# Performance work log

Measured on AMD Instinct MI355X. Metric: run time of the kernel, lower is better.

The kernel has to match this reference:

```python
import jax, jax.numpy as jnp
import numpy as np

EPS = 1e-5  # torch LayerNorm default


def _layernorm_hd(t, gamma, beta):
    # Normalize jointly over the last two axes (n_heads, head_dim),
    # matching nn.LayerNorm((n_heads, head_dim)).
    mu = jnp.mean(t, axis=(-2, -1), keepdims=True)
    var = jnp.var(t, axis=(-2, -1), keepdims=True)
    return (t - mu) * jax.lax.rsqrt(var + EPS) * gamma + beta


def setup_inputs() -> dict:
    key = jax.random.key(0)
    B, Hs, Ws, C = 4, 256, 256, 128  # batch, spatial grid, hidden_channels
    n_heads, head_dim = 4, C // 4
    scale = (C ** 2) / n_heads  # hidden_channels**2 / n_heads, as in __init__
    ks = jax.random.split(key, 4)
    X = jax.random.normal(ks[0], (B, Hs, Ws, C), dtype=jnp.float32)
    Wq = jax.random.normal(ks[1], (C, n_heads, head_dim), dtype=jnp.float32) / scale
    Wk = jax.random.normal(ks[2], (C, n_heads, head_dim), dtype=jnp.float32) / scale
    Wv = jax.random.normal(ks[3], (C, n_heads, head_dim), dtype=jnp.float32) / scale
    # NOTE: original forward applies layernorm_key to BOTH key and value
    # (layernorm_value params are unused); we replicate that exactly.
    gamma_k = jnp.ones((n_heads, head_dim), dtype=jnp.float32)
    beta_k = jnp.zeros((n_heads, head_dim), dtype=jnp.float32)
    return {"X": X, "Wq": Wq, "Wk": Wk, "Wv": Wv, "gamma_k": gamma_k, "beta_k": beta_k}


def reference(X, Wq, Wk, Wv, gamma_k, beta_k):
    # X: [B, Hs, Ws, C]; W*: [C, h, d]
    q = jnp.einsum('bxyc,chd->bxyhd', X, Wq)
    k = jnp.einsum('bxyc,chd->bxyhd', X, Wk)
    v = jnp.einsum('bxyc,chd->bxyhd', X, Wv)
    k = _layernorm_hd(k, gamma_k, beta_k)
    v = _layernorm_hd(v, gamma_k, beta_k)  # faithful: layernorm_key used for value too
    num_points = X.shape[1] * X.shape[2]
    kv = jnp.einsum('bxyhd,bxyhe->bhde', k, v)          # tiny [B,h,d,d]
    sa = jnp.einsum('bxyhd,bhde->bxyeh', q, kv)          # note output order (e, h)
    sa = (sa / num_points).reshape(X.shape)
    return sa
```

## Files before the change

kernel.cpp:

```cpp
#include <hip/hip_runtime.h>

#define HW 65536
#define CH 128
#define NHEADS 4
#define HDIM 32
#define EPS 1e-5f
#define INV_NP (1.0f / 65536.0f)
#define INV_C (1.0f / 128.0f)

typedef float v4f __attribute__((ext_vector_type(4)));
typedef short v8s __attribute__((ext_vector_type(8)));
typedef unsigned int v4u __attribute__((ext_vector_type(4)));

__device__ __forceinline__ ushort f2bf(float f) {
    uint u = __float_as_uint(f);
    return (ushort)((u + 0x7FFFu + ((u >> 16) & 1u)) >> 16);
}

__device__ __forceinline__ uint cvtpk(float lo, float hi) {
    uint r;
    asm("v_cvt_pk_bf16_f32 %0, %1, %2" : "=v"(r) : "v"(lo), "v"(hi));
    return r;
}

__device__ __forceinline__ v8s pack8(const float4& a, const float4& b) {
    union { uint u[4]; v8s s; } r;
    r.u[0] = cvtpk(a.x, a.y);
    r.u[1] = cvtpk(a.z, a.w);
    r.u[2] = cvtpk(b.x, b.y);
    r.u[3] = cvtpk(b.z, b.w);
    return r.s;
}

template<int CTRL>
__device__ __forceinline__ float dppadd(float x) {
    return x + __int_as_float(
        __builtin_amdgcn_mov_dpp(__float_as_int(x), CTRL, 0xF, 0xF, true));
}
__device__ __forceinline__ float red16(float x) {
    x = dppadd<0xB1>(x);
    x = dppadd<0x4E>(x);
    x = dppadd<0x141>(x);
    x = dppadd<0x140>(x);
    return x;
}

#define MFMA(a, b, c) __builtin_amdgcn_mfma_f32_16x16x32_bf16((a), (b), (c), 0, 0, 0)


__global__ __launch_bounds__(256) void prep_kernel(const float* __restrict__ Wk,
                                                   const float* __restrict__ Wv,
                                                   ushort* __restrict__ SWkT,
                                                   ushort* __restrict__ SWvT,
                                                   float* __restrict__ kv_g) {
    const int t = blockIdx.x * 256 + threadIdx.x;
    kv_g[t] = 0.f;
    kv_g[t + 8192] = 0.f;
#pragma unroll
    for (int i = 0; i < 2; ++i) {
        const int e = i * 8192 + t;
        const int c = e >> 7;
        const int row = e & 127;
        const int dst = row * 128 + (((c >> 3) + row) & 15) * 8 + (c & 7);
        SWkT[dst] = f2bf(Wk[e]);
        SWvT[dst] = f2bf(Wv[e]);
    }
}

__global__ __launch_bounds__(256, 2) void kv_kernel(const float* __restrict__ X,
                                                    const ushort* __restrict__ SWkT,
                                                    const ushort* __restrict__ SWvT,
                                                    const float* __restrict__ gamma,
                                                    const float* __restrict__ beta,
                                                    float* __restrict__ kv_g) {
    __shared__ ushort lds[40960];
    const int tid  = threadIdx.x;
    const int lane = tid & 63;
    const int w    = tid >> 6;
    const int q    = lane >> 4;
    const int ln   = lane & 15;

    const int batch  = blockIdx.x >> 7;
    const int blocal = blockIdx.x & 127;
    const float* Xb = X + ((size_t)batch * HW + (size_t)blocal * 512) * CH;

    {
        const v4u* sk = (const v4u*)SWkT;
        const v4u* sv = (const v4u*)SWvT;
        v4u* dk = (v4u*)lds;
        v4u* dv = (v4u*)(lds + 16384);
#pragma unroll
        for (int n = 0; n < 8; ++n) {
            dk[n * 256 + tid] = sk[n * 256 + tid];
            dv[n * 256 + tid] = sv[n * 256 + tid];
        }
    }

    float g8[8], be8[8];
#pragma unroll
    for (int ct = 0; ct < 8; ++ct) {
        g8[ct]  = gamma[ct * 16 + ln];
        be8[ct] = beta[ct * 16 + ln];
    }

    int brow[8];
#pragma unroll
    for (int ct = 0; ct < 8; ++ct) brow[ct] = (ct * 16 + ln) * 128;
    int bks[4];
#pragma unroll
    for (int ks = 0; ks < 4; ++ks) bks[ks] = ((ks * 4 + q + ln) & 15) * 8;
    int soff[8];
#pragma unroll
    for (int ct = 0; ct < 8; ++ct) {
        const int chn  = ct * 16 + ln;
        const int slot = (((w & 1) << 1) + (q >> 1) + chn) & 3;
        soff[ct] = chn * 32 + slot * 8 + (q & 1) * 4;
    }
    const int r0 = w * 32 + ln;
    const int r1 = r0 + 16;
    const int koff0 = r0 * 32 + ((q + r0) & 3) * 8;
    const int koff1 = r1 * 32 + ((q + r1) & 3) * 8;

    v4f kv00 = {0.f, 0.f, 0.f, 0.f}, kv01 = kv00, kv10 = kv00, kv11 = kv00;

    const float* xbase = Xb + (w * 16 + ln) * CH + q * 8;
    float4 xa[8];
#pragma unroll
    for (int ks = 0; ks < 4; ++ks) {
        xa[2 * ks]     = *(const float4*)(xbase + ks * 32);
        xa[2 * ks + 1] = *(const float4*)(xbase + ks * 32 + 4);
    }
    __syncthreads();

    v8s A[4];
#pragma unroll
    for (int ks = 0; ks < 4; ++ks) A[ks] = pack8(xa[2 * ks], xa[2 * ks + 1]);

    for (int t = 0; t < 8; ++t) {
        if (t < 7) {
            const float* xp = xbase + (size_t)(t + 1) * 64 * CH;
#pragma unroll
            for (int ks = 0; ks < 4; ++ks) {
                xa[2 * ks]     = *(const float4*)(xp + ks * 32);
                xa[2 * ks + 1] = *(const float4*)(xp + ks * 32 + 4);
            }
        }

        v4f ak[8], av[8];
#pragma unroll
        for (int ct = 0; ct < 8; ++ct) {
            ak[ct] = (v4f){0.f, 0.f, 0.f, 0.f};
            av[ct] = (v4f){0.f, 0.f, 0.f, 0.f};
        }
#pragma unroll
        for (int ks = 0; ks < 4; ++ks) {
#pragma unroll
            for (int ct = 0; ct < 8; ++ct) {
                const int kb = brow[ct] + bks[ks];
                const v8s Bk = *(const v8s*)(lds + kb);
                const v8s Bv = *(const v8s*)(lds + 16384 + kb);
                ak[ct] = MFMA(A[ks], Bk, ak[ct]);
                av[ct] = MFMA(A[ks], Bv, av[ct]);
            }
        }

        float rsk[4], rsv[4], mrk[4], mrv[4];
#pragma unroll
        for (int r = 0; r < 4; ++r) {
            float sk = 0.f, qk = 0.f, sv = 0.f, qv = 0.f;
#pragma unroll
            for (int ct = 0; ct < 8; ++ct) {
                sk += ak[ct][r]; qk = fmaf(ak[ct][r], ak[ct][r], qk);
                sv += av[ct][r]; qv = fmaf(av[ct][r], av[ct][r], qv);
            }
            sk = red16(sk); qk = red16(qk);
            sv = red16(sv); qv = red16(qv);
            const float mk = sk * INV_C, mv = sv * INV_C;
            const float rk = __builtin_amdgcn_rsqf(fmaf(qk, INV_C, -mk * mk) + EPS);
            const float rv = __builtin_amdgcn_rsqf(fmaf(qv, INV_C, -mv * mv) + EPS);
            rsk[r] = rk; mrk[r] = mk * rk;
            rsv[r] = rv; mrv[r] = mv * rv;
        }

#pragma unroll
        for (int rnd = 0; rnd < 2; ++rnd) {
            if ((w >> 1) == rnd) {
#pragma unroll
                for (int ct = 0; ct < 8; ++ct) {
#pragma unroll
                    for (int r = 0; r < 4; r += 2) {
                        const float k0 = fmaf(fmaf(ak[ct][r],     rsk[r],     -mrk[r]),     g8[ct], be8[ct]);
                        const float k1 = fmaf(fmaf(ak[ct][r + 1], rsk[r + 1], -mrk[r + 1]), g8[ct], be8[ct]);
                        const float v0 = fmaf(fmaf(av[ct][r],     rsv[r],     -mrv[r]),     g8[ct], be8[ct]);
                        const float v1 = fmaf(fmaf(av[ct][r + 1], rsv[r + 1], -mrv[r + 1]), g8[ct], be8[ct]);
                        *(uint*)(lds + 32768 + soff[ct] + r) = cvtpk(k0, k1);
                        *(uint*)(lds + 36864 + soff[ct] + r) = cvtpk(v0, v1);
                    }
                }
            }
            __syncthreads();
            {
                const v8s Ad0 = *(const v8s*)(lds + 32768 + koff0);
                const v8s Ad1 = *(const v8s*)(lds + 32768 + koff1);
                const v8s Be0 = *(const v8s*)(lds + 36864 + koff0);
                const v8s Be1 = *(const v8s*)(lds + 36864 + koff1);
                kv00 = MFMA(Ad0, Be0, kv00);
                kv01 = MFMA(Ad0, Be1, kv01);
                kv10 = MFMA(Ad1, Be0, kv10);
                kv11 = MFMA(Ad1, Be1, kv11);
            }
            __syncthreads();
        }

        if (t < 7) {
#pragma unroll
            for (int ks = 0; ks < 4; ++ks) A[ks] = pack8(xa[2 * ks], xa[2 * ks + 1]);
        }
    }

    float* dst = kv_g + (batch * NHEADS + w) * (HDIM * HDIM);
#pragma unroll
    for (int dt = 0; dt < 2; ++dt)
#pragma unroll
        for (int et = 0; et < 2; ++et) {
            const v4f f = dt == 0 ? (et == 0 ? kv00 : kv01) : (et == 0 ? kv10 : kv11);
#pragma unroll
            for (int r = 0; r < 4; ++r) {
                const int d = dt * 16 + q * 4 + r;
                const int e = et * 16 + ln;
                atomicAdd(&dst[d * HDIM + e], f[r]);
            }
        }
}

__global__ __launch_bounds__(256) void weff_kernel(const float* __restrict__ Wq,
                                                   const float* __restrict__ kv_g,
                                                   ushort* __restrict__ SWeffT) {
    const int b = blockIdx.x >> 4;
    const int part = blockIdx.x & 15;
    const int base = part * 1024 + threadIdx.x * 4;
    const int c = base >> 7;
    const int o0 = base & 127;
    const float* kvb = kv_g + b * (NHEADS * HDIM * HDIM);
#pragma unroll
    for (int n = 0; n < 4; ++n) {
        const int o = o0 + n;
        const int h = o & 3;
        const int e = o >> 2;
        float s = 0.f;
#pragma unroll
        for (int d = 0; d < HDIM; ++d)
            s += Wq[c * CH + h * HDIM + d] * kvb[h * (HDIM * HDIM) + d * HDIM + e];
        SWeffT[b * (CH * CH) + o * 128 + (((c >> 3) + o) & 15) * 8 + (c & 7)] = f2bf(s * INV_NP);
    }
}

__global__ __launch_bounds__(256, 4) void out_kernel(const float* __restrict__ X,
                                                     const ushort* __restrict__ SWeffT,
                                                     float* __restrict__ out) {
    __shared__ ushort lds[16384];
    const int tid  = threadIdx.x;
    const int lane = tid & 63;
    const int w    = tid >> 6;
    const int q    = lane >> 4;
    const int ln   = lane & 15;

    const int batch  = blockIdx.x >> 8;
    const int blocal = blockIdx.x & 255;
    const size_t p0 = (size_t)batch * HW + (size_t)blocal * 256;

    {
        const v4u* s = (const v4u*)(SWeffT + batch * (CH * CH));
        v4u* d = (v4u*)lds;
#pragma unroll
        for (int n = 0; n < 8; ++n) d[n * 256 + tid] = s[n * 256 + tid];
    }

    int arow[8];
#pragma unroll
    for (int ot = 0; ot < 8; ++ot) arow[ot] = (ot * 16 + ln) * 128;
    int aks[4];
#pragma unroll
    for (int ks = 0; ks < 4; ++ks) aks[ks] = ((ks * 4 + q + ln) & 15) * 8;

    const float* xbase = X + (p0 + w * 16 + ln) * CH + q * 8;
    float* obase       = out + (p0 + w * 16 + ln) * CH + q * 4;

    float4 xa[8];
#pragma unroll
    for (int ks = 0; ks < 4; ++ks) {
        xa[2 * ks]     = *(const float4*)(xbase + ks * 32);
        xa[2 * ks + 1] = *(const float4*)(xbase + ks * 32 + 4);
    }
    __syncthreads();

    v8s Bx[4];
#pragma unroll
    for (int ks = 0; ks < 4; ++ks) Bx[ks] = pack8(xa[2 * ks], xa[2 * ks + 1]);

    for (int t = 0; t < 4; ++t) {
        if (t < 3) {
            const float* xp = xbase + (size_t)(t + 1) * 64 * CH;
#pragma unroll
            for (int ks = 0; ks < 4; ++ks) {
                xa[2 * ks]     = *(const float4*)(xp + ks * 32);
                xa[2 * ks + 1] = *(const float4*)(xp + ks * 32 + 4);
            }
        }

        v4f acc[8];
#pragma unroll
        for (int ot = 0; ot < 8; ++ot) acc[ot] = (v4f){0.f, 0.f, 0.f, 0.f};
#pragma unroll
        for (int ks = 0; ks < 4; ++ks) {
#pragma unroll
            for (int ot = 0; ot < 8; ++ot) {
                const v8s Aw = *(const v8s*)(lds + arow[ot] + aks[ks]);
                acc[ot] = MFMA(Aw, Bx[ks], acc[ot]);
            }
        }

        float* op = obase + (size_t)t * 64 * CH;
#pragma unroll
        for (int ot = 0; ot < 8; ++ot) {
            float4 s;
            s.x = acc[ot][0]; s.y = acc[ot][1]; s.z = acc[ot][2]; s.w = acc[ot][3];
            *(float4*)(op + ot * 16) = s;
        }

        if (t < 3) {
#pragma unroll
            for (int ks = 0; ks < 4; ++ks) Bx[ks] = pack8(xa[2 * ks], xa[2 * ks + 1]);
        }
    }
}

extern "C" void kernel_launch(void* const* d_in, const int* in_sizes, int n_in,
                              void* d_out, int out_size, void* d_ws, size_t ws_size,
                              hipStream_t stream) {
    const float* X     = (const float*)d_in[0];
    const float* Wq    = (const float*)d_in[1];
    const float* Wk    = (const float*)d_in[2];
    const float* Wv    = (const float*)d_in[3];
    const float* gamma = (const float*)d_in[4];
    const float* beta  = (const float*)d_in[5];
    float* out = (float*)d_out;

    float*  kv_g   = (float*)d_ws;
    ushort* SWkT   = (ushort*)((char*)d_ws + 65536);
    ushort* SWvT   = (ushort*)((char*)d_ws + 98304);
    ushort* SWeffT = (ushort*)((char*)d_ws + 131072);

    prep_kernel<<<32, 256, 0, stream>>>(Wk, Wv, SWkT, SWvT, kv_g);
    kv_kernel<<<512, 256, 0, stream>>>(X, SWkT, SWvT, gamma, beta, kv_g);
    weff_kernel<<<64, 256, 0, stream>>>(Wq, kv_g, SWeffT);
    out_kernel<<<1024, 256, 0, stream>>>(X, SWeffT, out);
}
```

Before: 279.1 us.

## Restructure kv_kernel: register-resident weight fragments, X staged in LDS, 8 waves

The K/V projection kernel now keeps pre-swizzled bf16 weight fragments in registers, so each wave owns a 32-channel slice of K or V, and X tiles are staged through double-buffered LDS. Previously every wave held all weights in LDS and reloaded them per MFMA. Blocks grow to 512 threads with a much smaller LDS footprint, which should allow higher occupancy. LayerNorm statistics are now reduced across waves through a shared scratch area, which adds extra barriers per tile. prep_kernel is rewritten to emit the weight data directly in MFMA fragment order.

```diff
diff --git a/kernel.cpp b/kernel.cpp
--- a/kernel.cpp
+++ b/kernel.cpp
@@ -47,33 +47,35 @@
 
 #define MFMA(a, b, c) __builtin_amdgcn_mfma_f32_16x16x32_bf16((a), (b), (c), 0, 0, 0)
 
-
 __global__ __launch_bounds__(256) void prep_kernel(const float* __restrict__ Wk,
                                                    const float* __restrict__ Wv,
-                                                   ushort* __restrict__ SWkT,
-                                                   ushort* __restrict__ SWvT,
+                                                   ushort* __restrict__ SWfrag,
                                                    float* __restrict__ kv_g) {
     const int t = blockIdx.x * 256 + threadIdx.x;
     kv_g[t] = 0.f;
     kv_g[t + 8192] = 0.f;
 #pragma unroll
-    for (int i = 0; i < 2; ++i) {
-        const int e = i * 8192 + t;
-        const int c = e >> 7;
-        const int row = e & 127;
-        const int dst = row * 128 + (((c >> 3) + row) & 15) * 8 + (c & 7);
-        SWkT[dst] = f2bf(Wk[e]);
-        SWvT[dst] = f2bf(Wv[e]);
-    }
-}
-
-__global__ __launch_bounds__(256, 2) void kv_kernel(const float* __restrict__ X,
-                                                    const ushort* __restrict__ SWkT,
-                                                    const ushort* __restrict__ SWvT,
+    for (int i = 0; i < 4; ++i) {
+        const int o = i * 8192 + t;
+        const int f = o >> 9;
+        const int lane = (o >> 3) & 63;
+        const int j = o & 7;
+        const int w = f >> 3;
+        const int ks = (f >> 1) & 3;
+        const int ct = f & 1;
+        const int col = (w & 3) * 32 + ct * 16 + (lane & 15);
+        const int c = ks * 32 + (lane >> 4) * 8 + j;
+        const float s = (w < 4 ? Wk : Wv)[c * CH + col];
+        SWfrag[o] = f2bf(s);
+    }
+}
+
+__global__ __launch_bounds__(512, 4) void kv_kernel(const float* __restrict__ X,
+                                                    const ushort* __restrict__ SWfrag,
                                                     const float* __restrict__ gamma,
                                                     const float* __restrict__ beta,
                                                     float* __restrict__ kv_g) {
-    __shared__ ushort lds[40960];
+    __shared__ ushort lds[17408];
     const int tid  = threadIdx.x;
     const int lane = tid & 63;
     const int w    = tid >> 6;
@@ -84,153 +86,149 @@
     const int blocal = blockIdx.x & 127;
     const float* Xb = X + ((size_t)batch * HW + (size_t)blocal * 512) * CH;
 
-    {
-        const v4u* sk = (const v4u*)SWkT;
-        const v4u* sv = (const v4u*)SWvT;
-        v4u* dk = (v4u*)lds;
-        v4u* dv = (v4u*)(lds + 16384);
-#pragma unroll
-        for (int n = 0; n < 8; ++n) {
-            dk[n * 256 + tid] = sk[n * 256 + tid];
-            dv[n * 256 + tid] = sv[n * 256 + tid];
-        }
-    }
-
-    float g8[8], be8[8];
-#pragma unroll
-    for (int ct = 0; ct < 8; ++ct) {
-        g8[ct]  = gamma[ct * 16 + ln];
-        be8[ct] = beta[ct * 16 + ln];
-    }
-
-    int brow[8];
-#pragma unroll
-    for (int ct = 0; ct < 8; ++ct) brow[ct] = (ct * 16 + ln) * 128;
-    int bks[4];
-#pragma unroll
-    for (int ks = 0; ks < 4; ++ks) bks[ks] = ((ks * 4 + q + ln) & 15) * 8;
-    int soff[8];
-#pragma unroll
-    for (int ct = 0; ct < 8; ++ct) {
-        const int chn  = ct * 16 + ln;
-        const int slot = (((w & 1) << 1) + (q >> 1) + chn) & 3;
-        soff[ct] = chn * 32 + slot * 8 + (q & 1) * 4;
-    }
-    const int r0 = w * 32 + ln;
-    const int r1 = r0 + 16;
-    const int koff0 = r0 * 32 + ((q + r0) & 3) * 8;
-    const int koff1 = r1 * 32 + ((q + r1) & 3) * 8;
-
-    v4f kv00 = {0.f, 0.f, 0.f, 0.f}, kv01 = kv00, kv10 = kv00, kv11 = kv00;
-
-    const float* xbase = Xb + (w * 16 + ln) * CH + q * 8;
-    float4 xa[8];
-#pragma unroll
-    for (int ks = 0; ks < 4; ++ks) {
-        xa[2 * ks]     = *(const float4*)(xbase + ks * 32);
-        xa[2 * ks + 1] = *(const float4*)(xbase + ks * 32 + 4);
-    }
+    v8s Bf[4][2];
+#pragma unroll
+    for (int ks = 0; ks < 4; ++ks)
+#pragma unroll
+        for (int ct = 0; ct < 2; ++ct)
+            Bf[ks][ct] = *(const v8s*)(SWfrag + ((w * 8 + ks * 2 + ct) * 512 + lane * 8));
+
+    const int cb = (w & 3) * 32;
+    float g2[2], be2[2];
+#pragma unroll
+    for (int ct = 0; ct < 2; ++ct) {
+        g2[ct]  = gamma[cb + ct * 16 + ln];
+        be2[ct] = beta[cb + ct * 16 + ln];
+    }
+
+    const int jrow = tid >> 4;
+    const int qt   = tid & 15;
+    const float* xptr = Xb + jrow * CH + qt * 8;
+    const int sdst = jrow * 128 + ((qt + jrow) & 15) * 8;
+    int aoff[4];
+#pragma unroll
+    for (int ks = 0; ks < 4; ++ks) aoff[ks] = ((ks * 4 + q + ln) & 15) * 8;
+    const int rowb0 = ln * 128;
+    const int rowb1 = (16 + ln) * 128;
+    const int tbase = (w < 4) ? 8192 : 12288;
+    int soff[2][2];
+#pragma unroll
+    for (int ct = 0; ct < 2; ++ct)
+#pragma unroll
+        for (int rt = 0; rt < 2; ++rt) {
+            const int chn  = cb + ct * 16 + ln;
+            const int slot = (rt * 2 + (q >> 1) + chn) & 3;
+            soff[ct][rt] = tbase + chn * 32 + slot * 8 + (q & 1) * 4;
+        }
+    const int h  = w >> 1;
+    const int eh = w & 1;
+    const int sl = (q + ln) & 3;
+    const int koff0 = 8192  + (h * 32 + ln) * 32 + sl * 8;
+    const int koff1 = 8192  + (h * 32 + 16 + ln) * 32 + sl * 8;
+    const int voff  = 12288 + (h * 32 + eh * 16 + ln) * 32 + sl * 8;
+    float* S = (float*)(lds + 16384);
+    const int tens = w >> 2;
+
+    v4f kv0 = {0.f, 0.f, 0.f, 0.f}, kv1 = kv0;
+
+    float4 xa0 = *(const float4*)xptr;
+    float4 xa1 = *(const float4*)(xptr + 4);
+    *(v8s*)(lds + sdst) = pack8(xa0, xa1);
     __syncthreads();
 
-    v8s A[4];
-#pragma unroll
-    for (int ks = 0; ks < 4; ++ks) A[ks] = pack8(xa[2 * ks], xa[2 * ks + 1]);
-
-    for (int t = 0; t < 8; ++t) {
-        if (t < 7) {
-            const float* xp = xbase + (size_t)(t + 1) * 64 * CH;
-#pragma unroll
-            for (int ks = 0; ks < 4; ++ks) {
-                xa[2 * ks]     = *(const float4*)(xp + ks * 32);
-                xa[2 * ks + 1] = *(const float4*)(xp + ks * 32 + 4);
-            }
-        }
-
-        v4f ak[8], av[8];
-#pragma unroll
-        for (int ct = 0; ct < 8; ++ct) {
-            ak[ct] = (v4f){0.f, 0.f, 0.f, 0.f};
-            av[ct] = (v4f){0.f, 0.f, 0.f, 0.f};
-        }
+    for (int t = 0; t < 16; ++t) {
+        if (t < 15) {
+            const float* xp = xptr + (size_t)(t + 1) * 32 * CH;
+            xa0 = *(const float4*)xp;
+            xa1 = *(const float4*)(xp + 4);
+        }
+        const int cur = (t & 1) * 4096;
+
+        v4f acc[2][2];
+#pragma unroll
+        for (int rt = 0; rt < 2; ++rt)
+#pragma unroll
+            for (int ct = 0; ct < 2; ++ct) acc[rt][ct] = (v4f){0.f, 0.f, 0.f, 0.f};
 #pragma unroll
         for (int ks = 0; ks < 4; ++ks) {
-#pragma unroll
-            for (int ct = 0; ct < 8; ++ct) {
-                const int kb = brow[ct] + bks[ks];
-                const v8s Bk = *(const v8s*)(lds + kb);
-                const v8s Bv = *(const v8s*)(lds + 16384 + kb);
-                ak[ct] = MFMA(A[ks], Bk, ak[ct]);
-                av[ct] = MFMA(A[ks], Bv, av[ct]);
-            }
-        }
-
-        float rsk[4], rsv[4], mrk[4], mrv[4];
+            const v8s A0 = *(const v8s*)(lds + cur + rowb0 + aoff[ks]);
+            const v8s A1 = *(const v8s*)(lds + cur + rowb1 + aoff[ks]);
+            acc[0][0] = MFMA(A0, Bf[ks][0], acc[0][0]);
+            acc[0][1] = MFMA(A0, Bf[ks][1], acc[0][1]);
+            acc[1][0] = MFMA(A1, Bf[ks][0], acc[1][0]);
+            acc[1][1] = MFMA(A1, Bf[ks][1], acc[1][1]);
+        }
+
+#pragma unroll
+        for (int rt = 0; rt < 2; ++rt)
+#pragma unroll
+            for (int r = 0; r < 4; ++r) {
+                float s  = acc[rt][0][r] + acc[rt][1][r];
+                float sq = fmaf(acc[rt][0][r], acc[rt][0][r],
+                                acc[rt][1][r] * acc[rt][1][r]);
+                s  = red16(s);
+                sq = red16(sq);
+                if (ln == 0) {
+                    const int pos = rt * 16 + q * 4 + r;
+                    *(float2*)(S + (tens * 32 + pos) * 8 + (w & 3) * 2) =
+                        make_float2(s, sq);
+                }
+            }
+        __syncthreads();
+
+        if (t < 15) *(v8s*)(lds + (cur ^ 4096) + sdst) = pack8(xa0, xa1);
+
+        float mr[2][4], rs[2][4];
+#pragma unroll
+        for (int rt = 0; rt < 2; ++rt)
+#pragma unroll
+            for (int r = 0; r < 4; ++r) {
+                const int pos = rt * 16 + q * 4 + r;
+                const float4 f0 = *(const float4*)(S + (tens * 32 + pos) * 8);
+                const float4 f1 = *(const float4*)(S + (tens * 32 + pos) * 8 + 4);
+                const float s  = f0.x + f0.z + f1.x + f1.z;
+                const float sq = f0.y + f0.w + f1.y + f1.w;
+                const float mu = s * INV_C;
+                const float rv = __builtin_amdgcn_rsqf(fmaf(sq, INV_C, -mu * mu) + EPS);
+                rs[rt][r] = rv;
+                mr[rt][r] = mu * rv;
+            }
+
+#pragma unroll
+        for (int ct = 0; ct < 2; ++ct)
+#pragma unroll
+            for (int rt = 0; rt < 2; ++rt) {
+                const float n0 = fmaf(fmaf(acc[rt][ct][0], rs[rt][0], -mr[rt][0]), g2[ct], be2[ct]);
+                const float n1 = fmaf(fmaf(acc[rt][ct][1], rs[rt][1], -mr[rt][1]), g2[ct], be2[ct]);
+                const float n2 = fmaf(fmaf(acc[rt][ct][2], rs[rt][2], -mr[rt][2]), g2[ct], be2[ct]);
+                const float n3 = fmaf(fmaf(acc[rt][ct][3], rs[rt][3], -mr[rt][3]), g2[ct], be2[ct]);
+                uint2 u;
+                u.x = cvtpk(n0, n1);
+                u.y = cvtpk(n2, n3);
+                *(uint2*)(lds + soff[ct][rt]) = u;
+            }
+        __syncthreads();
+
+        {
+            const v8s Ad0 = *(const v8s*)(lds + koff0);
+            const v8s Ad1 = *(const v8s*)(lds + koff1);
+            const v8s Be  = *(const v8s*)(lds + voff);
+            kv0 = MFMA(Ad0, Be, kv0);
+            kv1 = MFMA(Ad1, Be, kv1);
+        }
+    }
+
+    float* dst = kv_g + (batch * NHEADS + h) * (HDIM * HDIM);
+#pragma unroll
+    for (int db = 0; db < 2; ++db) {
+        const v4f f = db == 0 ? kv0 : kv1;
 #pragma unroll
         for (int r = 0; r < 4; ++r) {
-            float sk = 0.f, qk = 0.f, sv = 0.f, qv = 0.f;
-#pragma unroll
-            for (int ct = 0; ct < 8; ++ct) {
-                sk += ak[ct][r]; qk = fmaf(ak[ct][r], ak[ct][r], qk);
-                sv += av[ct][r]; qv = fmaf(av[ct][r], av[ct][r], qv);
-            }
-            sk = red16(sk); qk = red16(qk);
-            sv = red16(sv); qv = red16(qv);
-            const float mk = sk * INV_C, mv = sv * INV_C;
-            const float rk = __builtin_amdgcn_rsqf(fmaf(qk, INV_C, -mk * mk) + EPS);
-            const float rv = __builtin_amdgcn_rsqf(fmaf(qv, INV_C, -mv * mv) + EPS);
-            rsk[r] = rk; mrk[r] = mk * rk;
-            rsv[r] = rv; mrv[r] = mv * rv;
-        }
-
-#pragma unroll
-        for (int rnd = 0; rnd < 2; ++rnd) {
-            if ((w >> 1) == rnd) {
-#pragma unroll
-                for (int ct = 0; ct < 8; ++ct) {
-#pragma unroll
-                    for (int r = 0; r < 4; r += 2) {
-                        const float k0 = fmaf(fmaf(ak[ct][r],     rsk[r],     -mrk[r]),     g8[ct], be8[ct]);
-                        const float k1 = fmaf(fmaf(ak[ct][r + 1], rsk[r + 1], -mrk[r + 1]), g8[ct], be8[ct]);
-                        const float v0 = fmaf(fmaf(av[ct][r],     rsv[r],     -mrv[r]),     g8[ct], be8[ct]);
-                        const float v1 = fmaf(fmaf(av[ct][r + 1], rsv[r + 1], -mrv[r + 1]), g8[ct], be8[ct]);
-                        *(uint*)(lds + 32768 + soff[ct] + r) = cvtpk(k0, k1);
-                        *(uint*)(lds + 36864 + soff[ct] + r) = cvtpk(v0, v1);
-                    }
-                }
-            }
-            __syncthreads();
-            {
-                const v8s Ad0 = *(const v8s*)(lds + 32768 + koff0);
-                const v8s Ad1 = *(const v8s*)(lds + 32768 + koff1);
-                const v8s Be0 = *(const v8s*)(lds + 36864 + koff0);
-                const v8s Be1 = *(const v8s*)(lds + 36864 + koff1);
-                kv00 = MFMA(Ad0, Be0, kv00);
-                kv01 = MFMA(Ad0, Be1, kv01);
-                kv10 = MFMA(Ad1, Be0, kv10);
-                kv11 = MFMA(Ad1, Be1, kv11);
-            }
-            __syncthreads();
-        }
-
-        if (t < 7) {
-#pragma unroll
-            for (int ks = 0; ks < 4; ++ks) A[ks] = pack8(xa[2 * ks], xa[2 * ks + 1]);
-        }
-    }
-
-    float* dst = kv_g + (batch * NHEADS + w) * (HDIM * HDIM);
-#pragma unroll
-    for (int dt = 0; dt < 2; ++dt)
-#pragma unroll
-        for (int et = 0; et < 2; ++et) {
-            const v4f f = dt == 0 ? (et == 0 ? kv00 : kv01) : (et == 0 ? kv10 : kv11);
-#pragma unroll
-            for (int r = 0; r < 4; ++r) {
-                const int d = dt * 16 + q * 4 + r;
-                const int e = et * 16 + ln;
-                atomicAdd(&dst[d * HDIM + e], f[r]);
-            }
-        }
+            const int d = db * 16 + q * 4 + r;
+            const int e = eh * 16 + ln;
+            atomicAdd(&dst[d * HDIM + e], f[r]);
+        }
+    }
 }
 
 __global__ __launch_bounds__(256) void weff_kernel(const float* __restrict__ Wq,
@@ -347,12 +345,11 @@
     float* out = (float*)d_out;
 
     float*  kv_g   = (float*)d_ws;
-    ushort* SWkT   = (ushort*)((char*)d_ws + 65536);
-    ushort* SWvT   = (ushort*)((char*)d_ws + 98304);
+    ushort* SWfrag = (ushort*)((char*)d_ws + 65536);
     ushort* SWeffT = (ushort*)((char*)d_ws + 131072);
 
-    prep_kernel<<<32, 256, 0, stream>>>(Wk, Wv, SWkT, SWvT, kv_g);
-    kv_kernel<<<512, 256, 0, stream>>>(X, SWkT, SWvT, gamma, beta, kv_g);
+    prep_kernel<<<32, 256, 0, stream>>>(Wk, Wv, SWfrag, kv_g);
+    kv_kernel<<<512, 512, 0, stream>>>(X, SWfrag, gamma, beta, kv_g);
     weff_kernel<<<64, 256, 0, stream>>>(Wq, kv_g, SWeffT);
     out_kernel<<<1024, 256, 0, stream>>>(X, SWeffT, out);
 }
```

New measurement: 277.4 us. No clear change (-0.6%).
